# Optimization experiments

Measured on AMD Instinct MI355X. Metric: run time of the kernel, lower is better.

## Reference

```python
import jax, jax.numpy as jnp
import numpy as np

B = 4096
C = 32000

def setup_inputs() -> dict:
    key = jax.random.key(0)
    k1, k2 = jax.random.split(key)
    output = jax.random.normal(k1, (B, C), dtype=jnp.float32)
    target = jax.random.randint(k2, (B,), 0, C, dtype=jnp.int64)
    return {"output": output, "target": target}

def reference(output, target):
    # probs: [B, C]
    probs = jax.nn.softmax(output, axis=1)
    batch_size, num_classes = probs.shape
    avg_conf = jnp.mean(probs, axis=0)  # [C]
    # avg_count[c] = mean(target == c)  == bincount(target)/B, fused scatter-add
    counts = jnp.zeros((num_classes,), dtype=probs.dtype).at[target].add(1.0)
    avg_count = counts / batch_size
    loss_mdca = jnp.mean(jnp.abs(avg_conf - avg_count))
    return loss_mdca
```

## Files before the change

### kernel.cpp

```cpp
#include <hip/hip_runtime.h>

#define BB 4096
#define CC 32000
#define CPAD 32768
#define NT 512
#define NI 16
#define GRID 256
#define RPB (BB / GRID)
#define FBLK 128

typedef float v4f __attribute__((ext_vector_type(4)));

__global__ __launch_bounds__(NT, 2) void mdca_main(const float* __restrict__ x,
                                                   const int* __restrict__ tgt,
                                                   float* __restrict__ partial,
                                                   float* __restrict__ counts) {
    __shared__ float acc[CPAD];
    __shared__ float red[NT / 64];
    __shared__ float s_rcp;

    const int t = threadIdx.x;
    const int r0 = blockIdx.x * RPB;

    for (int i = t; i < CPAD / 4; i += NT) ((v4f*)acc)[i] = (v4f){0.f, 0.f, 0.f, 0.f};

    v4f cur[NI], nxt[NI];

    {
        const float* rp = x + (size_t)r0 * CC;
#pragma unroll
        for (int i = 0; i < NI; ++i) {
            const int col = i * 2048 + 4 * t;
            if (col < CC) cur[i] = __builtin_nontemporal_load((const v4f*)(rp + col));
        }
    }
    __syncthreads();

    for (int r = 0; r < RPB; ++r) {
        if (r + 1 < RPB) {
            const float* rp = x + (size_t)(r0 + r + 1) * CC;
#pragma unroll
            for (int i = 0; i < NI; ++i) {
                const int col = i * 2048 + 4 * t;
                if (col < CC) nxt[i] = __builtin_nontemporal_load((const v4f*)(rp + col));
            }
        }
        float s = 0.f;
#pragma unroll
        for (int i = 0; i < NI; ++i) {
            const int col = i * 2048 + 4 * t;
            if (col < CC) {
                v4f e;
                e.x = __expf(cur[i].x); e.y = __expf(cur[i].y);
                e.z = __expf(cur[i].z); e.w = __expf(cur[i].w);
                cur[i] = e;
                s += e.x + e.y + e.z + e.w;
            }
        }
        for (int off = 32; off > 0; off >>= 1) s += __shfl_down(s, off);
        if ((t & 63) == 0) red[t >> 6] = s;
        __syncthreads();
        if (t == 0) {
            float z = 0.f;
#pragma unroll
            for (int w = 0; w < NT / 64; ++w) z += red[w];
            s_rcp = 1.0f / z;
        }
        __syncthreads();
        const float rz = s_rcp;
#pragma unroll
        for (int i = 0; i < NI; ++i) {
            const int col = i * 2048 + 4 * t;
            if (col < CC) {
                v4f a = ((v4f*)acc)[i * 512 + t];
                a.x += cur[i].x * rz; a.y += cur[i].y * rz;
                a.z += cur[i].z * rz; a.w += cur[i].w * rz;
                ((v4f*)acc)[i * 512 + t] = a;
            }
        }
        if (r + 1 < RPB) {
#pragma unroll
            for (int i = 0; i < NI; ++i) cur[i] = nxt[i];
        }
    }

    v4f* pp = (v4f*)(partial + (size_t)blockIdx.x * CPAD);
#pragma unroll
    for (int i = 0; i < NI; ++i) {
        const int col = i * 2048 + 4 * t;
        v4f a = (col < CC) ? ((v4f*)acc)[i * 512 + t] : (v4f){0.f, 0.f, 0.f, 0.f};
        pp[i * 512 + t] = a;
    }
    if (t < RPB) atomicAdd(&counts[tgt[r0 + t]], 1.0f);
}

__global__ __launch_bounds__(256) void finalize(const float* __restrict__ partial,
                                                const float* __restrict__ counts,
                                                float* __restrict__ total,
                                                unsigned* __restrict__ blkcnt,
                                                float* __restrict__ out) {
    const int g = blockIdx.x * 256 + threadIdx.x;
    v4f s = {0.f, 0.f, 0.f, 0.f};
    const v4f* pv = (const v4f*)partial;
    for (int b = 0; b < GRID; ++b) {
        v4f p = pv[(size_t)b * (CPAD / 4) + g];
        s.x += p.x; s.y += p.y; s.z += p.z; s.w += p.w;
    }
    float v = 0.f;
    const int c = 4 * g;
    if (c < CC) {
        v4f cnt = *(const v4f*)(counts + c);
        v = fabsf(s.x - cnt.x) + fabsf(s.y - cnt.y) + fabsf(s.z - cnt.z) + fabsf(s.w - cnt.w);
    }
    for (int off = 32; off > 0; off >>= 1) v += __shfl_down(v, off);
    __shared__ float wsum[4];
    if ((threadIdx.x & 63) == 0) wsum[threadIdx.x >> 6] = v;
    __syncthreads();
    if (threadIdx.x == 0) {
        atomicAdd(total, wsum[0] + wsum[1] + wsum[2] + wsum[3]);
        __threadfence();
        unsigned prev = atomicAdd(blkcnt, 1u);
        if (prev == FBLK - 1) {
            float tot = atomicAdd(total, 0.0f);
            out[0] = tot * (1.0f / ((float)BB * (float)CC));
        }
    }
}

extern "C" void kernel_launch(void* const* d_in, const int* in_sizes, int n_in,
                              void* d_out, int out_size, void* d_ws, size_t ws_size,
                              hipStream_t stream) {
    const float* x = (const float*)d_in[0];
    const int* tgt = (const int*)d_in[1];
    float* out = (float*)d_out;

    float* partial = (float*)d_ws;
    float* counts = partial + (size_t)GRID * CPAD;
    float* total = counts + CC;
    unsigned* blkcnt = (unsigned*)(total + 1);

    (void)hipMemsetAsync(counts, 0, (size_t)(CC + 2) * 4, stream);

    mdca_main<<<GRID, NT, 0, stream>>>(x, tgt, partial, counts);
    finalize<<<FBLK, 256, 0, stream>>>(partial, counts, total, blkcnt, out);
}
```

Baseline: 658.8 us.

## Keep per-column softmax accumulators in registers with 1024-thread blocks

Replaces the 128 KB shared-memory column accumulator with per-thread register accumulators. Blocks grow to 1024 threads so each thread owns 8 float4 columns. The row reduction now uses a double-buffered shared array so every thread computes the reciprocal itself, which removes one barrier per row. Nontemporal loads are dropped and the finalize loop is unrolled. The intent is to remove LDS read-modify-write traffic and the LDS occupancy limit, at the cost of higher register pressure.

```diff
diff --git a/kernel.cpp b/kernel.cpp
--- a/kernel.cpp
+++ b/kernel.cpp
@@ -3,53 +3,54 @@
 #define BB 4096
 #define CC 32000
 #define CPAD 32768
-#define NT 512
-#define NI 16
+#define NT 1024
+#define NI 8
 #define GRID 256
 #define RPB (BB / GRID)
-#define FBLK 128
+#define NW (NT / 64)
+#define FBLK (CPAD / 4 / 256)
 
 typedef float v4f __attribute__((ext_vector_type(4)));
 
-__global__ __launch_bounds__(NT, 2) void mdca_main(const float* __restrict__ x,
+__global__ __launch_bounds__(NT, 4) void mdca_main(const float* __restrict__ x,
                                                    const int* __restrict__ tgt,
                                                    float* __restrict__ partial,
                                                    float* __restrict__ counts) {
-    __shared__ float acc[CPAD];
-    __shared__ float red[NT / 64];
-    __shared__ float s_rcp;
+    __shared__ float red[2][NW];
 
     const int t = threadIdx.x;
+    const int wid = t >> 6;
     const int r0 = blockIdx.x * RPB;
 
-    for (int i = t; i < CPAD / 4; i += NT) ((v4f*)acc)[i] = (v4f){0.f, 0.f, 0.f, 0.f};
+    const bool tail_ok = ((NI - 1) * (NT * 4) + 4 * t) < CC;
 
-    v4f cur[NI], nxt[NI];
+    v4f cur[NI], nxt[NI], acc[NI];
+#pragma unroll
+    for (int i = 0; i < NI; ++i) acc[i] = (v4f){0.f, 0.f, 0.f, 0.f};
 
     {
         const float* rp = x + (size_t)r0 * CC;
 #pragma unroll
         for (int i = 0; i < NI; ++i) {
-            const int col = i * 2048 + 4 * t;
-            if (col < CC) cur[i] = __builtin_nontemporal_load((const v4f*)(rp + col));
+            const int col = i * (NT * 4) + 4 * t;
+            if (i < NI - 1 || tail_ok) cur[i] = *(const v4f*)(rp + col);
         }
     }
-    __syncthreads();
 
     for (int r = 0; r < RPB; ++r) {
+        const int p = r & 1;
         if (r + 1 < RPB) {
-            const float* rp = x + (size_t)(r0 + r + 1) * CC;
+            const float* rq = x + (size_t)(r0 + r + 1) * CC;
 #pragma unroll
             for (int i = 0; i < NI; ++i) {
-                const int col = i * 2048 + 4 * t;
-                if (col < CC) nxt[i] = __builtin_nontemporal_load((const v4f*)(rp + col));
+                const int col = i * (NT * 4) + 4 * t;
+                if (i < NI - 1 || tail_ok) nxt[i] = *(const v4f*)(rq + col);
             }
         }
         float s = 0.f;
 #pragma unroll
         for (int i = 0; i < NI; ++i) {
-            const int col = i * 2048 + 4 * t;
-            if (col < CC) {
+            if (i < NI - 1 || tail_ok) {
                 v4f e;
                 e.x = __expf(cur[i].x); e.y = __expf(cur[i].y);
                 e.z = __expf(cur[i].z); e.w = __expf(cur[i].w);
@@ -58,24 +59,17 @@
             }
         }
         for (int off = 32; off > 0; off >>= 1) s += __shfl_down(s, off);
-        if ((t & 63) == 0) red[t >> 6] = s;
+        if ((t & 63) == 0) red[p][wid] = s;
         __syncthreads();
-        if (t == 0) {
-            float z = 0.f;
+        float z = 0.f;
 #pragma unroll
-            for (int w = 0; w < NT / 64; ++w) z += red[w];
-            s_rcp = 1.0f / z;
-        }
-        __syncthreads();
-        const float rz = s_rcp;
+        for (int w = 0; w < NW; ++w) z += red[p][w];
+        const float rz = 1.0f / z;
 #pragma unroll
         for (int i = 0; i < NI; ++i) {
-            const int col = i * 2048 + 4 * t;
-            if (col < CC) {
-                v4f a = ((v4f*)acc)[i * 512 + t];
-                a.x += cur[i].x * rz; a.y += cur[i].y * rz;
-                a.z += cur[i].z * rz; a.w += cur[i].w * rz;
-                ((v4f*)acc)[i * 512 + t] = a;
+            if (i < NI - 1 || tail_ok) {
+                acc[i].x += cur[i].x * rz; acc[i].y += cur[i].y * rz;
+                acc[i].z += cur[i].z * rz; acc[i].w += cur[i].w * rz;
             }
         }
         if (r + 1 < RPB) {
@@ -86,11 +80,8 @@
 
     v4f* pp = (v4f*)(partial + (size_t)blockIdx.x * CPAD);
 #pragma unroll
-    for (int i = 0; i < NI; ++i) {
-        const int col = i * 2048 + 4 * t;
-        v4f a = (col < CC) ? ((v4f*)acc)[i * 512 + t] : (v4f){0.f, 0.f, 0.f, 0.f};
-        pp[i * 512 + t] = a;
-    }
+    for (int i = 0; i < NI; ++i) pp[i * NT + t] = acc[i];
+
     if (t < RPB) atomicAdd(&counts[tgt[r0 + t]], 1.0f);
 }
 
@@ -102,6 +93,7 @@
     const int g = blockIdx.x * 256 + threadIdx.x;
     v4f s = {0.f, 0.f, 0.f, 0.f};
     const v4f* pv = (const v4f*)partial;
+#pragma unroll 4
     for (int b = 0; b < GRID; ++b) {
         v4f p = pv[(size_t)b * (CPAD / 4) + g];
         s.x += p.x; s.y += p.y; s.z += p.z; s.w += p.w;
```

New measurement: 688.7 us. 1.05x slower.
